# Kernel tuning notes

Measured on AMD Instinct MI355X. Metric: run time of the kernel, lower is better.

The kernel has to match this reference:

```python
import jax, jax.numpy as jnp
import numpy as np

BLOCK = 128          # block_size in the source
FP8_MAX = 448.0      # max representable magnitude of float8_e4m3fn


def _quant_weight(w):
    """Pre-quantize a [N, K] float weight into fp8 values + per 128x128 block scales."""
    N, K = w.shape
    wb = w.reshape(N // BLOCK, BLOCK, K // BLOCK, BLOCK)
    w_scale = jnp.max(jnp.abs(wb), axis=(1, 3)) / FP8_MAX           # [Nb, Kb]
    s = jnp.where(w_scale == 0, 1.0, w_scale)
    wq = (wb / s[:, None, :, None]).astype(jnp.float8_e4m3fn).astype(jnp.float32)
    return wq.reshape(N, K), w_scale


def setup_inputs() -> dict:
    key = jax.random.key(0)
    kx, kw = jax.random.split(key)
    M, K, N = 16384, 2048, 2048
    x = jax.random.normal(kx, (M, K), dtype=jnp.float32)
    w = jax.random.normal(kw, (N, K), dtype=jnp.float32) * 0.02
    w_fp8, w_scale = _quant_weight(w)
    return {"x": x, "w_fp8": w_fp8, "w_scale": w_scale}


def reference(x, w_fp8, w_scale):
    """fp8 block-quantized linear: act_quant(x) then dequantized GEMM.

    x:       [M, K] float32 activations
    w_fp8:   [N, K] fp8-valued weight (stored as float32, exactly e4m3 representable)
    w_scale: [N/128, K/128] per-block weight scales
    """
    M, K = x.shape
    N = w_fp8.shape[0]
    # --- act_quant: per 128-element block along K, scale = amax / 448 ---
    xb = x.reshape(M, K // BLOCK, BLOCK)
    x_scale = jnp.max(jnp.abs(xb), axis=-1) / FP8_MAX               # [M, Kb]
    sx = jnp.where(x_scale == 0, 1.0, x_scale)
    xq = (xb / sx[..., None]).astype(jnp.float8_e4m3fn).astype(jnp.float32)
    # --- fp8_gemm with inline dequant: scales factor out per (m-block, n-block, k-block)
    # sum_kb sx[m,kb]*sw[nb,kb]*(xq . wq) == (xq*sx) @ (wq*sw)^T exactly ---
    x_deq = (xq * sx[..., None]).reshape(M, K)
    w_deq = (w_fp8.reshape(N // BLOCK, BLOCK, K // BLOCK, BLOCK)
             * w_scale[:, None, :, None]).reshape(N, K)
    return x_deq @ w_deq.T                                          # [M, N]
```

## Files before the change

kernel.cpp:

```cpp
#include <hip/hip_runtime.h>

#define M_DIM 16384
#define N_DIM 2048
#define K_DIM 2048
#define KB    (K_DIM / 128)

#define BM 256
#define BN 256
#define BK 64
#define NT (K_DIM / BK)

#define XGRID (M_DIM * K_DIM / 2048)
#define WGRID (N_DIM * K_DIM / 2048)

typedef __bf16 bf16x8 __attribute__((ext_vector_type(8)));
typedef float  f32x4  __attribute__((ext_vector_type(4)));

__device__ __forceinline__ unsigned short f32_to_bf16_rne(float f) {
    unsigned int u = __float_as_uint(f);
    u += 0x7FFFu + ((u >> 16) & 1u);
    return (unsigned short)(u >> 16);
}

__global__ __launch_bounds__(256) void quant_all_kernel(const float* __restrict__ x,
                                                        unsigned short* __restrict__ xdq,
                                                        const float* __restrict__ w,
                                                        const float* __restrict__ wscale,
                                                        unsigned short* __restrict__ wdq) {
    const int tid = threadIdx.x;
    if (blockIdx.x < XGRID) {
        const size_t base = ((size_t)blockIdx.x * 256 + tid) * 8;
        const float4 va = *(const float4*)(x + base);
        const float4 vb = *(const float4*)(x + base + 4);
        float amax = fmaxf(
            fmaxf(fmaxf(fabsf(va.x), fabsf(va.y)), fmaxf(fabsf(va.z), fabsf(va.w))),
            fmaxf(fmaxf(fabsf(vb.x), fabsf(vb.y)), fmaxf(fabsf(vb.z), fabsf(vb.w))));
#pragma unroll
        for (int m = 8; m >= 1; m >>= 1)
            amax = fmaxf(amax, __shfl_xor(amax, m, 64));
        float s = amax / 448.0f;
        if (s == 0.0f) s = 1.0f;
        const int p01 = __builtin_amdgcn_cvt_pk_fp8_f32(va.x / s, va.y / s, 0, false);
        const int p23 = __builtin_amdgcn_cvt_pk_fp8_f32(va.z / s, va.w / s, 0, false);
        const int p45 = __builtin_amdgcn_cvt_pk_fp8_f32(vb.x / s, vb.y / s, 0, false);
        const int p67 = __builtin_amdgcn_cvt_pk_fp8_f32(vb.z / s, vb.w / s, 0, false);
        uint4 out;
        out.x = (unsigned int)f32_to_bf16_rne(__builtin_amdgcn_cvt_f32_fp8(p01, 0) * s)
              | ((unsigned int)f32_to_bf16_rne(__builtin_amdgcn_cvt_f32_fp8(p01, 1) * s) << 16);
        out.y = (unsigned int)f32_to_bf16_rne(__builtin_amdgcn_cvt_f32_fp8(p23, 0) * s)
              | ((unsigned int)f32_to_bf16_rne(__builtin_amdgcn_cvt_f32_fp8(p23, 1) * s) << 16);
        out.z = (unsigned int)f32_to_bf16_rne(__builtin_amdgcn_cvt_f32_fp8(p45, 0) * s)
              | ((unsigned int)f32_to_bf16_rne(__builtin_amdgcn_cvt_f32_fp8(p45, 1) * s) << 16);
        out.w = (unsigned int)f32_to_bf16_rne(__builtin_amdgcn_cvt_f32_fp8(p67, 0) * s)
              | ((unsigned int)f32_to_bf16_rne(__builtin_amdgcn_cvt_f32_fp8(p67, 1) * s) << 16);
        *(uint4*)(xdq + base) = out;
    } else {
        const size_t e = ((size_t)(blockIdx.x - XGRID) * 256 + tid) * 8;
        const float4 va = *(const float4*)(w + e);
        const float4 vb = *(const float4*)(w + e + 4);
        const int n = (int)(e >> 11);
        const int k = (int)(e & 2047);
        const float s = wscale[(n >> 7) * KB + (k >> 7)];
        uint4 out;
        out.x = (unsigned int)f32_to_bf16_rne(va.x * s) | ((unsigned int)f32_to_bf16_rne(va.y * s) << 16);
        out.y = (unsigned int)f32_to_bf16_rne(va.z * s) | ((unsigned int)f32_to_bf16_rne(va.w * s) << 16);
        out.z = (unsigned int)f32_to_bf16_rne(vb.x * s) | ((unsigned int)f32_to_bf16_rne(vb.y * s) << 16);
        out.w = (unsigned int)f32_to_bf16_rne(vb.z * s) | ((unsigned int)f32_to_bf16_rne(vb.w * s) << 16);
        *(uint4*)(wdq + e) = out;
    }
}

__global__ __launch_bounds__(512, 2) void gemm_bt_kernel(const unsigned short* __restrict__ A,
                                                         const unsigned short* __restrict__ B,
                                                         float* __restrict__ C) {
    __shared__ __align__(16) unsigned short As[2][2][256][32];
    __shared__ __align__(16) unsigned short Bs[2][2][256][32];

    const int tid  = threadIdx.x;
    const int lane = tid & 63;
    const int wave = tid >> 6;
    const int wm   = (wave >> 2) * 128;
    const int wn   = (wave & 3) * 64;
    const int quad = lane >> 4;
    const int l16  = lane & 15;
    const int pc   = quad ^ ((l16 >> 1) & 3);

    const int m0 = blockIdx.x * BM;
    const int n0 = blockIdx.y * BN;

    f32x4 acc[8][4] = {};

    const int srow = tid >> 2;
    const int sc   = (tid & 3) ^ ((tid >> 3) & 3);
    const unsigned short* gA = A + (size_t)(m0 + srow) * K_DIM + sc * 8;
    const unsigned short* gB = B + (size_t)(n0 + srow) * K_DIM + sc * 8;

#define GLD(SRC, DST) __builtin_amdgcn_global_load_lds( \
    (__attribute__((address_space(1))) void*)(SRC), \
    (__attribute__((address_space(3))) void*)(DST), 16, 0, 0)

#define STAGE4(BUF, KH, KT) do { \
    GLD(gA + (size_t)(KT) * 64 + (KH) * 32,                       &As[BUF][KH][wave * 16][0]); \
    GLD(gA + (size_t)128 * K_DIM + (size_t)(KT) * 64 + (KH) * 32, &As[BUF][KH][128 + wave * 16][0]); \
    GLD(gB + (size_t)(KT) * 64 + (KH) * 32,                       &Bs[BUF][KH][wave * 16][0]); \
    GLD(gB + (size_t)128 * K_DIM + (size_t)(KT) * 64 + (KH) * 32, &Bs[BUF][KH][128 + wave * 16][0]); \
  } while (0)

#define VMCNT(n) asm volatile("s_waitcnt vmcnt(" #n ")" ::: "memory")
#define BAR() __builtin_amdgcn_s_barrier()

#define PHASE(BUF, KK, WAIT, STAGES) do { \
    STAGES; \
    bf16x8 af[8], bfr[4]; \
    _Pragma("unroll") \
    for (int i = 0; i < 8; ++i) \
      af[i] = *(const bf16x8*)(&As[BUF][KK][wm + i * 16 + l16][pc * 8]); \
    _Pragma("unroll") \
    for (int j = 0; j < 4; ++j) \
      bfr[j] = *(const bf16x8*)(&Bs[BUF][KK][wn + j * 16 + l16][pc * 8]); \
    __builtin_amdgcn_s_setprio(1); \
    _Pragma("unroll") \
    for (int i = 0; i < 8; ++i) { \
      _Pragma("unroll") \
      for (int j = 0; j < 4; ++j) \
        acc[i][j] = __builtin_amdgcn_mfma_f32_16x16x32_bf16(af[i], bfr[j], acc[i][j], 0, 0, 0); \
    } \
    __builtin_amdgcn_s_setprio(0); \
    WAIT; \
    BAR(); \
  } while (0)

    STAGE4(0, 0, 0);
    STAGE4(0, 1, 0);
    STAGE4(1, 0, 1);
    VMCNT(8);
    BAR();

#pragma unroll 1
    for (int t = 0; t < NT - 2; t += 2) {
        PHASE(0, 0, VMCNT(8), STAGE4(1, 1, t + 1));
        PHASE(0, 1, VMCNT(8), STAGE4(0, 0, t + 2));
        PHASE(1, 0, VMCNT(8), STAGE4(0, 1, t + 2));
        PHASE(1, 1, VMCNT(8), STAGE4(1, 0, t + 3));
    }
    PHASE(0, 0, VMCNT(8), STAGE4(1, 1, NT - 1));
    PHASE(0, 1, VMCNT(4), (void)0);
    PHASE(1, 0, VMCNT(0), (void)0);
    PHASE(1, 1, (void)0, (void)0);

#pragma unroll
    for (int i = 0; i < 8; ++i) {
        const int row = m0 + wm + i * 16 + quad * 4;
#pragma unroll
        for (int j = 0; j < 4; ++j) {
            const int col = n0 + wn + j * 16 + l16;
            float* cp = C + (size_t)row * N_DIM + col;
#pragma unroll
            for (int r = 0; r < 4; ++r)
                cp[(size_t)r * N_DIM] = acc[i][j][r];
        }
    }
}

extern "C" void kernel_launch(void* const* d_in, const int* in_sizes, int n_in,
                              void* d_out, int out_size, void* d_ws, size_t ws_size,
                              hipStream_t stream) {
    const float* x      = (const float*)d_in[0];
    const float* wfp8   = (const float*)d_in[1];
    const float* wscale = (const float*)d_in[2];
    float* out = (float*)d_out;

    unsigned short* xdq = (unsigned short*)d_ws;
    unsigned short* wdq = xdq + (size_t)M_DIM * K_DIM;

    quant_all_kernel<<<XGRID + WGRID, 256, 0, stream>>>(x, xdq, wfp8, wscale, wdq);
    gemm_bt_kernel<<<dim3(M_DIM / BM, N_DIM / BN), 512, 0, stream>>>(xdq, wdq, out);
}
```

Measured before the change: 371.1 us.

## Split GEMM k-phases into half-phases interleaving staging loads with MFMA blocks

Each 32-wide k-slice is now processed in two halves of 8x2 MFMAs. The A-tile and B-tile global-to-LDS loads are issued separately, one before each half, with barriers placed around every MFMA block. Only two B fragments are kept live at a time, which lowers register pressure and spreads memory issue more evenly between compute bursts. The cost is roughly four times as many workgroup barriers per k-step, which could add stall time.

New measurement: 363.1 us. 1.02x faster.

```diff
diff --git a/kernel.cpp b/kernel.cpp
--- a/kernel.cpp
+++ b/kernel.cpp
@@ -99,54 +99,62 @@
     (__attribute__((address_space(1))) void*)(SRC), \
     (__attribute__((address_space(3))) void*)(DST), 16, 0, 0)
 
-#define STAGE4(BUF, KH, KT) do { \
-    GLD(gA + (size_t)(KT) * 64 + (KH) * 32,                       &As[BUF][KH][wave * 16][0]); \
-    GLD(gA + (size_t)128 * K_DIM + (size_t)(KT) * 64 + (KH) * 32, &As[BUF][KH][128 + wave * 16][0]); \
-    GLD(gB + (size_t)(KT) * 64 + (KH) * 32,                       &Bs[BUF][KH][wave * 16][0]); \
-    GLD(gB + (size_t)128 * K_DIM + (size_t)(KT) * 64 + (KH) * 32, &Bs[BUF][KH][128 + wave * 16][0]); \
+#define STG_A(DB, KH, KT) do { \
+    GLD(gA + (size_t)(KT) * 64 + (KH) * 32,                       &As[DB][KH][wave * 16][0]); \
+    GLD(gA + (size_t)128 * K_DIM + (size_t)(KT) * 64 + (KH) * 32, &As[DB][KH][128 + wave * 16][0]); \
+  } while (0)
+#define STG_B(DB, KH, KT) do { \
+    GLD(gB + (size_t)(KT) * 64 + (KH) * 32,                       &Bs[DB][KH][wave * 16][0]); \
+    GLD(gB + (size_t)128 * K_DIM + (size_t)(KT) * 64 + (KH) * 32, &Bs[DB][KH][128 + wave * 16][0]); \
   } while (0)
 
 #define VMCNT(n) asm volatile("s_waitcnt vmcnt(" #n ")" ::: "memory")
 #define BAR() __builtin_amdgcn_s_barrier()
 
-#define PHASE(BUF, KK, WAIT, STAGES) do { \
-    STAGES; \
-    bf16x8 af[8], bfr[4]; \
-    _Pragma("unroll") \
-    for (int i = 0; i < 8; ++i) \
-      af[i] = *(const bf16x8*)(&As[BUF][KK][wm + i * 16 + l16][pc * 8]); \
-    _Pragma("unroll") \
-    for (int j = 0; j < 4; ++j) \
-      bfr[j] = *(const bf16x8*)(&Bs[BUF][KK][wn + j * 16 + l16][pc * 8]); \
+#define LDA(BUF, KK, i) (*(const bf16x8*)(&As[BUF][KK][wm + (i) * 16 + l16][pc * 8]))
+#define LDB(BUF, KK, j) (*(const bf16x8*)(&Bs[BUF][KK][wn + (j) * 16 + l16][pc * 8]))
+
+#define MM8x2(J0, B0, B1) do { \
     __builtin_amdgcn_s_setprio(1); \
     _Pragma("unroll") \
     for (int i = 0; i < 8; ++i) { \
-      _Pragma("unroll") \
-      for (int j = 0; j < 4; ++j) \
-        acc[i][j] = __builtin_amdgcn_mfma_f32_16x16x32_bf16(af[i], bfr[j], acc[i][j], 0, 0, 0); \
+      acc[i][J0]     = __builtin_amdgcn_mfma_f32_16x16x32_bf16(af[i], B0, acc[i][J0],     0, 0, 0); \
+      acc[i][(J0)+1] = __builtin_amdgcn_mfma_f32_16x16x32_bf16(af[i], B1, acc[i][(J0)+1], 0, 0, 0); \
     } \
     __builtin_amdgcn_s_setprio(0); \
-    WAIT; \
-    BAR(); \
   } while (0)
 
-    STAGE4(0, 0, 0);
-    STAGE4(0, 1, 0);
-    STAGE4(1, 0, 1);
+#define TILE(BUF, S0, S1, S2, S3, W1, W3) do { \
+    bf16x8 af[8], b0, b1; \
+    _Pragma("unroll") \
+    for (int i = 0; i < 8; ++i) af[i] = LDA(BUF, 0, i); \
+    b0 = LDB(BUF, 0, 0); b1 = LDB(BUF, 0, 1); \
+    S0; BAR(); MM8x2(0, b0, b1); BAR(); \
+    b0 = LDB(BUF, 0, 2); b1 = LDB(BUF, 0, 3); \
+    S1; BAR(); MM8x2(2, b0, b1); W1; BAR(); \
+    _Pragma("unroll") \
+    for (int i = 0; i < 8; ++i) af[i] = LDA(BUF, 1, i); \
+    b0 = LDB(BUF, 1, 0); b1 = LDB(BUF, 1, 1); \
+    S2; BAR(); MM8x2(0, b0, b1); BAR(); \
+    b0 = LDB(BUF, 1, 2); b1 = LDB(BUF, 1, 3); \
+    S3; BAR(); MM8x2(2, b0, b1); W3; BAR(); \
+  } while (0)
+
+    STG_A(0, 0, 0); STG_B(0, 0, 0);
+    STG_A(0, 1, 0); STG_B(0, 1, 0);
+    STG_A(1, 0, 1); STG_B(1, 0, 1);
     VMCNT(8);
     BAR();
 
 #pragma unroll 1
     for (int t = 0; t < NT - 2; t += 2) {
-        PHASE(0, 0, VMCNT(8), STAGE4(1, 1, t + 1));
-        PHASE(0, 1, VMCNT(8), STAGE4(0, 0, t + 2));
-        PHASE(1, 0, VMCNT(8), STAGE4(0, 1, t + 2));
-        PHASE(1, 1, VMCNT(8), STAGE4(1, 0, t + 3));
+        TILE(0, STG_A(1, 1, t + 1), STG_B(1, 1, t + 1),
+                STG_A(0, 0, t + 2), STG_B(0, 0, t + 2), VMCNT(8), VMCNT(8));
+        TILE(1, STG_A(0, 1, t + 2), STG_B(0, 1, t + 2),
+                STG_A(1, 0, t + 3), STG_B(1, 0, t + 3), VMCNT(8), VMCNT(8));
     }
-    PHASE(0, 0, VMCNT(8), STAGE4(1, 1, NT - 1));
-    PHASE(0, 1, VMCNT(4), (void)0);
-    PHASE(1, 0, VMCNT(0), (void)0);
-    PHASE(1, 1, (void)0, (void)0);
+    TILE(0, STG_A(1, 1, NT - 1), STG_B(1, 1, NT - 1), (void)0, (void)0, VMCNT(8), VMCNT(4));
+    TILE(1, (void)0, (void)0, (void)0, (void)0, VMCNT(0), (void)0);
 
 #pragma unroll
     for (int i = 0; i < 8; ++i) {
```

## Switch GEMM to 32x32x16 MFMA with 64-wide swizzled LDS and fragment double-buffering

Applied to the files above, without the earlier changes.

Replaces the 16x16x32 bf16 MFMA tiles with 32x32x16 MFMAs, so each wave issues fewer, larger matrix instructions and loads fewer LDS fragments per flop. The LDS layout becomes a single 64-column tile per buffer with an XOR swizzle over eight 16-byte chunks. The pipeline is restructured to prefetch the next k-slice's register fragments while the current MFMAs run. Global loads now use a plain two-stage double buffer with a full vmcnt(0) wait per tile, which may expose more global-load latency than the previous deeper staging.

New measurement: 361.0 us. 2.7% less time.

```diff
diff --git a/kernel.cpp b/kernel.cpp
--- a/kernel.cpp
+++ b/kernel.cpp
@@ -14,7 +14,7 @@
 #define WGRID (N_DIM * K_DIM / 2048)
 
 typedef __bf16 bf16x8 __attribute__((ext_vector_type(8)));
-typedef float  f32x4  __attribute__((ext_vector_type(4)));
+typedef float  f32x16 __attribute__((ext_vector_type(16)));
 
 __device__ __forceinline__ unsigned short f32_to_bf16_rne(float f) {
     unsigned int u = __float_as_uint(f);
@@ -73,25 +73,25 @@
 __global__ __launch_bounds__(512, 2) void gemm_bt_kernel(const unsigned short* __restrict__ A,
                                                          const unsigned short* __restrict__ B,
                                                          float* __restrict__ C) {
-    __shared__ __align__(16) unsigned short As[2][2][256][32];
-    __shared__ __align__(16) unsigned short Bs[2][2][256][32];
+    __shared__ __align__(16) unsigned short As[2][256][64];
+    __shared__ __align__(16) unsigned short Bs[2][256][64];
 
     const int tid  = threadIdx.x;
     const int lane = tid & 63;
     const int wave = tid >> 6;
     const int wm   = (wave >> 2) * 128;
     const int wn   = (wave & 3) * 64;
-    const int quad = lane >> 4;
-    const int l16  = lane & 15;
-    const int pc   = quad ^ ((l16 >> 1) & 3);
+    const int l32  = lane & 31;
+    const int hi   = lane >> 5;
+    const int swz  = l32 & 7;
 
     const int m0 = blockIdx.x * BM;
     const int n0 = blockIdx.y * BN;
 
-    f32x4 acc[8][4] = {};
+    f32x16 acc[4][2] = {};
 
-    const int srow = tid >> 2;
-    const int sc   = (tid & 3) ^ ((tid >> 3) & 3);
+    const int srow = tid >> 3;
+    const int sc   = (tid & 7) ^ (srow & 7);
     const unsigned short* gA = A + (size_t)(m0 + srow) * K_DIM + sc * 8;
     const unsigned short* gB = B + (size_t)(n0 + srow) * K_DIM + sc * 8;
 
@@ -99,65 +99,81 @@
     (__attribute__((address_space(1))) void*)(SRC), \
     (__attribute__((address_space(3))) void*)(DST), 16, 0, 0)
 
-#define STAGE4(BUF, KH, KT) do { \
-    GLD(gA + (size_t)(KT) * 64 + (KH) * 32,                       &As[BUF][KH][wave * 16][0]); \
-    GLD(gA + (size_t)128 * K_DIM + (size_t)(KT) * 64 + (KH) * 32, &As[BUF][KH][128 + wave * 16][0]); \
-    GLD(gB + (size_t)(KT) * 64 + (KH) * 32,                       &Bs[BUF][KH][wave * 16][0]); \
-    GLD(gB + (size_t)128 * K_DIM + (size_t)(KT) * 64 + (KH) * 32, &Bs[BUF][KH][128 + wave * 16][0]); \
+#define STG_A4(DB, KT) do { \
+    GLD(gA + (size_t)(KT) * 64,                        &As[DB][      wave * 8][0]); \
+    GLD(gA + (size_t) 64 * K_DIM + (size_t)(KT) * 64,  &As[DB][ 64 + wave * 8][0]); \
+    GLD(gA + (size_t)128 * K_DIM + (size_t)(KT) * 64,  &As[DB][128 + wave * 8][0]); \
+    GLD(gA + (size_t)192 * K_DIM + (size_t)(KT) * 64,  &As[DB][192 + wave * 8][0]); \
+  } while (0)
+#define STG_B4(DB, KT) do { \
+    GLD(gB + (size_t)(KT) * 64,                        &Bs[DB][      wave * 8][0]); \
+    GLD(gB + (size_t) 64 * K_DIM + (size_t)(KT) * 64,  &Bs[DB][ 64 + wave * 8][0]); \
+    GLD(gB + (size_t)128 * K_DIM + (size_t)(KT) * 64,  &Bs[DB][128 + wave * 8][0]); \
+    GLD(gB + (size_t)192 * K_DIM + (size_t)(KT) * 64,  &Bs[DB][192 + wave * 8][0]); \
   } while (0)
 
 #define VMCNT(n) asm volatile("s_waitcnt vmcnt(" #n ")" ::: "memory")
 #define BAR() __builtin_amdgcn_s_barrier()
 
-#define PHASE(BUF, KK, WAIT, STAGES) do { \
-    STAGES; \
-    bf16x8 af[8], bfr[4]; \
-    _Pragma("unroll") \
-    for (int i = 0; i < 8; ++i) \
-      af[i] = *(const bf16x8*)(&As[BUF][KK][wm + i * 16 + l16][pc * 8]); \
-    _Pragma("unroll") \
-    for (int j = 0; j < 4; ++j) \
-      bfr[j] = *(const bf16x8*)(&Bs[BUF][KK][wn + j * 16 + l16][pc * 8]); \
+    bf16x8 fa[2][4], fb[2][2];
+
+#define LDA32(BUF, KK, I) (*(const bf16x8*)(&As[BUF][wm + (I) * 32 + l32][(((KK) * 2 + hi) ^ swz) * 8]))
+#define LDB32(BUF, KK, J) (*(const bf16x8*)(&Bs[BUF][wn + (J) * 32 + l32][(((KK) * 2 + hi) ^ swz) * 8]))
+
+#define READK(P, BUF, KK) do { \
+    fa[P][0] = LDA32(BUF, KK, 0); fa[P][1] = LDA32(BUF, KK, 1); \
+    fa[P][2] = LDA32(BUF, KK, 2); fa[P][3] = LDA32(BUF, KK, 3); \
+    fb[P][0] = LDB32(BUF, KK, 0); fb[P][1] = LDB32(BUF, KK, 1); \
+  } while (0)
+
+#define MM(P) do { \
     __builtin_amdgcn_s_setprio(1); \
     _Pragma("unroll") \
-    for (int i = 0; i < 8; ++i) { \
-      _Pragma("unroll") \
-      for (int j = 0; j < 4; ++j) \
-        acc[i][j] = __builtin_amdgcn_mfma_f32_16x16x32_bf16(af[i], bfr[j], acc[i][j], 0, 0, 0); \
+    for (int i = 0; i < 4; ++i) { \
+      acc[i][0] = __builtin_amdgcn_mfma_f32_32x32x16_bf16(fa[P][i], fb[P][0], acc[i][0], 0, 0, 0); \
+      acc[i][1] = __builtin_amdgcn_mfma_f32_32x32x16_bf16(fa[P][i], fb[P][1], acc[i][1], 0, 0, 0); \
     } \
     __builtin_amdgcn_s_setprio(0); \
-    WAIT; \
-    BAR(); \
   } while (0)
 
-    STAGE4(0, 0, 0);
-    STAGE4(0, 1, 0);
-    STAGE4(1, 0, 1);
-    VMCNT(8);
+#define TILE_STD(B_, KTN) do { \
+    READK(1, B_, 1);        STG_A4((B_) ^ 1, KTN); MM(0); \
+    READK(0, B_, 2);        STG_B4((B_) ^ 1, KTN); MM(1); \
+    READK(1, B_, 3);        MM(0); VMCNT(0); BAR(); \
+    READK(0, (B_) ^ 1, 0);  MM(1); BAR(); \
+  } while (0)
+
+#define TILE_LAST(B_) do { \
+    READK(1, B_, 1); MM(0); \
+    READK(0, B_, 2); MM(1); \
+    READK(1, B_, 3); MM(0); \
+    MM(1); \
+  } while (0)
+
+    STG_A4(0, 0);
+    STG_B4(0, 0);
+    VMCNT(0);
     BAR();
+    READK(0, 0, 0);
 
 #pragma unroll 1
     for (int t = 0; t < NT - 2; t += 2) {
-        PHASE(0, 0, VMCNT(8), STAGE4(1, 1, t + 1));
-        PHASE(0, 1, VMCNT(8), STAGE4(0, 0, t + 2));
-        PHASE(1, 0, VMCNT(8), STAGE4(0, 1, t + 2));
-        PHASE(1, 1, VMCNT(8), STAGE4(1, 0, t + 3));
+        TILE_STD(0, t + 1);
+        TILE_STD(1, t + 2);
     }
-    PHASE(0, 0, VMCNT(8), STAGE4(1, 1, NT - 1));
-    PHASE(0, 1, VMCNT(4), (void)0);
-    PHASE(1, 0, VMCNT(0), (void)0);
-    PHASE(1, 1, (void)0, (void)0);
+    TILE_STD(0, NT - 1);
+    TILE_LAST(1);
 
 #pragma unroll
-    for (int i = 0; i < 8; ++i) {
-        const int row = m0 + wm + i * 16 + quad * 4;
+    for (int i = 0; i < 4; ++i) {
 #pragma unroll
-        for (int j = 0; j < 4; ++j) {
-            const int col = n0 + wn + j * 16 + l16;
-            float* cp = C + (size_t)row * N_DIM + col;
+        for (int j = 0; j < 2; ++j) {
+            const int col = n0 + wn + j * 32 + l32;
 #pragma unroll
-            for (int r = 0; r < 4; ++r)
-                cp[(size_t)r * N_DIM] = acc[i][j][r];
+            for (int r = 0; r < 16; ++r) {
+                const int row = m0 + wm + i * 32 + (r & 3) + 8 * (r >> 2) + 4 * hi;
+                C[(size_t)row * N_DIM + col] = acc[i][j][r];
+            }
         }
     }
 }
```
